# Kernel optimization log

Measured on AMD Instinct MI355X. Metric: run time of the kernel, lower is better.

Reference implementation:

```python
import jax, jax.numpy as jnp
import numpy as np

BOS_ID = 0
EOS_ID = 1


def setup_inputs() -> dict:
    key = jax.random.key(0)
    ks = jax.random.split(key, 16)
    B, L, F = 64, 200, 512
    H, E, A = 512, 512, 512
    V, T = 50257, 21
    D = E + F  # rnn input_dim
    s = lambda n: 1.0 / np.sqrt(n)
    ref = jax.random.randint(ks[0], (B, T), 2, V, dtype=jnp.int32)
    ref = ref.at[:, 0].set(BOS_ID).at[:, -1].set(EOS_ID)
    return {
        "encoder_output": jax.random.normal(ks[1], (B, L, F), jnp.float32),
        "decoder_init_hidden": jax.random.normal(ks[2], (1, B, H), jnp.float32),
        "encoding_mask": jnp.ones((B, L, 1), jnp.float32),
        "temp_seg": jax.random.uniform(ks[3], (B, 2), jnp.float32),
        "embed_table": jax.random.normal(ks[4], (V, E), jnp.float32) * 0.02,
        "W_ih": jax.random.normal(ks[5], (3 * H, D), jnp.float32) * s(D),
        "W_hh": jax.random.normal(ks[6], (3 * H, H), jnp.float32) * s(H),
        "b_ih": jnp.zeros((3 * H,), jnp.float32),
        "b_hh": jnp.zeros((3 * H,), jnp.float32),
        "Wa_enc": jax.random.normal(ks[7], (F, A), jnp.float32) * s(F),
        "Wa_h": jax.random.normal(ks[8], (H, A), jnp.float32) * s(H),
        "v_att": jax.random.normal(ks[9], (A,), jnp.float32) * s(A),
        "W_out": jax.random.normal(ks[10], (V, H), jnp.float32) * s(H),
        "b_out": jnp.zeros((V,), jnp.float32),
        "ref_caption": ref,
    }


def reference(encoder_output, decoder_init_hidden, encoding_mask, temp_seg,
              embed_table, W_ih, W_hh, b_ih, b_hh,
              Wa_enc, Wa_h, v_att, W_out, b_out, ref_caption):
    # Teacher-forced training forward of RNNSeqDecoder (GRU, 1 layer).
    B, T = ref_caption.shape
    V = embed_table.shape[0]
    enc_proj = jnp.einsum('blf,fa->bla', encoder_output, Wa_enc)  # precompute attn enc term
    mask = encoding_mask[..., 0]  # (B,L)
    h0 = decoder_init_hidden[0]   # (B,H)

    def step(h, word):
        emb = embed_table[word]                                        # (B,E)
        # additive attention over encoder states (masked)
        score = jnp.einsum('bla,a->bl', jnp.tanh(enc_proj + (h @ Wa_h)[:, None, :]), v_att)
        score = jnp.where(mask > 0, score, -1e9)
        attn = jax.nn.softmax(score, axis=1)
        ctx = jnp.einsum('bl,blf->bf', attn, encoder_output)           # (B,F)
        x = jnp.concatenate([emb, ctx], axis=1)                        # (B,E+F)
        # PyTorch GRU cell
        gi = x @ W_ih.T + b_ih
        gh = h @ W_hh.T + b_hh
        i_r, i_z, i_n = jnp.split(gi, 3, axis=1)
        h_r, h_z, h_n = jnp.split(gh, 3, axis=1)
        r = jax.nn.sigmoid(i_r + h_r)
        z = jax.nn.sigmoid(i_z + h_z)
        n = jnp.tanh(i_n + r * h_n)
        h_new = (1.0 - z) * n + z * h
        logp = jax.nn.log_softmax(h_new @ W_out.T + b_out, axis=1)     # (B,V)
        return h_new, logp

    _, logps = jax.lax.scan(step, h0, ref_caption[:, :-1].T)           # (T-1,B,V)
    first = jnp.zeros((B, 1, V), logps.dtype)  # BOS_ID == 0, matches torch.zeros(...) + BOS_ID
    caption_prob = jnp.concatenate([first, jnp.swapaxes(logps, 0, 1)], axis=1)  # (B,T,V)
    return caption_prob
```

## Files before the change

kernel.cpp:

```cpp
#include <hip/hip_runtime.h>
#include <stdint.h>
#include <stddef.h>

#define B_ 64
#define L_ 200
#define F_ 512
#define H_ 512
#define A_ 512
#define E_ 512
#define V_ 50257
#define PADV 50304
#define T_ 21
#define D_ 1024
#define NBLK_LOG 786
#define BH (B_ * H_)
#define BD (B_ * D_)
#define NROW 1280

typedef __attribute__((ext_vector_type(8))) short short8;
typedef __attribute__((ext_vector_type(4))) float f32x4;

__device__ __forceinline__ unsigned short f2b(float f) {
  unsigned int u = __builtin_bit_cast(unsigned int, f);
  u += 0x7FFFu + ((u >> 16) & 1u);
  return (unsigned short)(u >> 16);
}
__device__ __forceinline__ float b2f(unsigned short s) {
  unsigned int u = ((unsigned int)s) << 16;
  return __builtin_bit_cast(float, u);
}
__device__ __forceinline__ f32x4 mfma16(short8 a, short8 b, f32x4 c) {
  return __builtin_amdgcn_mfma_f32_16x16x32_bf16(a, b, c, 0, 0, 0);
}
__device__ __forceinline__ int hsoff(int b, int j) {
  return (((b >> 4) * 16 + (j >> 5)) * 64 + (((j >> 3) & 3) * 16 + (b & 15))) * 8 + (j & 7);
}
__device__ __forceinline__ int xoff(int b, int k) {
  return (((b >> 4) * 32 + (k >> 5)) * 64 + (((k >> 3) & 3) * 16 + (b & 15))) * 8 + (k & 7);
}


__global__ void k_cvt(const float* __restrict__ src, unsigned short* __restrict__ dst, int n4) {
  int i = blockIdx.x * blockDim.x + threadIdx.x;
  int stride = gridDim.x * blockDim.x;
  const float4* s4 = (const float4*)src;
  ushort4* d4 = (ushort4*)dst;
  for (; i < n4; i += stride) {
    float4 v = s4[i];
    ushort4 o;
    o.x = f2b(v.x); o.y = f2b(v.y); o.z = f2b(v.z); o.w = f2b(v.w);
    d4[i] = o;
  }
}

__global__ void k_wfrag(const float* __restrict__ src, unsigned short* __restrict__ dst, int K) {
  int rt = blockIdx.x;
  int r15 = threadIdx.x & 15;
  int row = rt * 16 + r15;
  int nch = K >> 3;
  int kpw = K >> 5;
  for (int kc = threadIdx.x >> 4; kc < nch; kc += 16) {
    const float4* s = (const float4*)(src + (size_t)row * K + kc * 8);
    float4 x = s[0], y = s[1];
    short8 o;
    o[0] = f2b(x.x); o[1] = f2b(x.y); o[2] = f2b(x.z); o[3] = f2b(x.w);
    o[4] = f2b(y.x); o[5] = f2b(y.y); o[6] = f2b(y.z); o[7] = f2b(y.w);
    *(short8*)(dst + ((size_t)(rt * kpw + (kc >> 2)) * 64 + ((kc & 3) * 16 + r15)) * 8) = o;
  }
}

__global__ void k_transcvt(const float* __restrict__ src, unsigned short* __restrict__ dst, int R, int C) {
  __shared__ float tile[64][65];
  int cb = blockIdx.x * 64, rb = blockIdx.y * 64;
  int tx = threadIdx.x & 63, ty = threadIdx.x >> 6;
#pragma unroll
  for (int i = 0; i < 16; ++i) {
    int r = ty * 16 + i;
    tile[r][tx] = src[(size_t)(rb + r) * C + cb + tx];
  }
  __syncthreads();
#pragma unroll
  for (int i = 0; i < 16; ++i) {
    int c = ty * 16 + i;
    dst[(size_t)(cb + c) * R + rb + tx] = f2b(tile[tx][c]);
  }
}

__global__ void k_trans32(const float* __restrict__ src, float* __restrict__ dst, int R, int C) {
  __shared__ float tile[64][65];
  int cb = blockIdx.x * 64, rb = blockIdx.y * 64;
  int tx = threadIdx.x & 63, ty = threadIdx.x >> 6;
#pragma unroll
  for (int i = 0; i < 16; ++i) {
    int r = ty * 16 + i;
    tile[r][tx] = src[(size_t)(rb + r) * C + cb + tx];
  }
  __syncthreads();
#pragma unroll
  for (int i = 0; i < 16; ++i) {
    int c = ty * 16 + i;
    dst[(size_t)(cb + c) * R + rb + tx] = tile[tx][c];
  }
}

__global__ void k_hs0(const float* __restrict__ src, unsigned short* __restrict__ hs) {
  int b = blockIdx.x;
  for (int j = threadIdx.x; j < H_; j += 256)
    hs[hsoff(b, j)] = f2b(src[(size_t)b * H_ + j]);
}

__global__ void k_embAll(const int* __restrict__ ref, const float* __restrict__ et,
                         unsigned short* __restrict__ xAll) {
  int b = blockIdx.x, tp = blockIdx.y;
  int word = ref[b * T_ + tp];
  const float* er = et + (size_t)word * E_;
  unsigned short* dst = xAll + (size_t)tp * BD;
  int c = threadIdx.x;
  const float4* s = (const float4*)(er + c * 8);
  float4 x = s[0], y = s[1];
  short8 o;
  o[0] = f2b(x.x); o[1] = f2b(x.y); o[2] = f2b(x.z); o[3] = f2b(x.w);
  o[4] = f2b(y.x); o[5] = f2b(y.y); o[6] = f2b(y.z); o[7] = f2b(y.w);
  *(short8*)(dst + xoff(b, c * 8)) = o;
}

__global__ __launch_bounds__(256, 2) void k_encproj2(const unsigned short* __restrict__ encb,
                                                     const unsigned short* __restrict__ WaTb,
                                                     unsigned short* __restrict__ epb) {
  __shared__ unsigned short al[32768];
  int tid = threadIdx.x;
  size_t rowbase = (size_t)blockIdx.x * 64;
  for (int idx = tid; idx < 4096; idx += 256) {
    int row = idx >> 6, seg = idx & 63;
    unsigned char* dp = (unsigned char*)al + row * 1024 + ((seg * 16) ^ ((row & 7) << 4));
    *(short8*)dp = *(const short8*)(encb + (rowbase + row) * F_ + seg * 8);
  }
  __syncthreads();
  int w = tid >> 6, lane = tid & 63, ln15 = lane & 15, g = lane >> 4;
  int sw = (ln15 & 7) << 4;
  const unsigned char* alb = (const unsigned char*)al;
  int mrow = w * 16 + ln15;
  for (int nt = 0; nt < 32; ++nt) {
    f32x4 acc = {0.f, 0.f, 0.f, 0.f};
    const unsigned short* brow = WaTb + (size_t)(nt * 16 + ln15) * F_ + 8 * g;
#pragma unroll 4
    for (int kk = 0; kk < 16; ++kk) {
      short8 bf = *(const short8*)(brow + kk * 32);
      short8 af = *(const short8*)(alb + mrow * 1024 + ((kk * 64 + 16 * g) ^ sw));
      acc = mfma16(af, bf, acc);
    }
#pragma unroll
    for (int r = 0; r < 4; ++r) {
      size_t m = rowbase + w * 16 + 4 * g + r;
      epb[m * A_ + nt * 16 + ln15] = f2b(acc[r]);
    }
  }
}

__global__ void k_zero0(float* __restrict__ out) {
  int b = blockIdx.y;
  float* o = out + (size_t)b * T_ * V_;
  int v0 = blockIdx.x * 1024 + threadIdx.x;
#pragma unroll
  for (int i = 0; i < 4; ++i) { int v = v0 + i * 256; if (v < V_) o[v] = 0.f; }
}


__global__ __launch_bounds__(256) void k_hw(const unsigned short* __restrict__ Wahf,
                                            const unsigned short* __restrict__ hs,
                                            float* __restrict__ hw) {
  int bx = blockIdx.x;
  int w = threadIdx.x >> 6, lane = threadIdx.x & 63;
  int ln15 = lane & 15, g = lane >> 4;
  f32x4 acc = {0.f, 0.f, 0.f, 0.f};
#pragma unroll 4
  for (int kk = 0; kk < 16; ++kk) {
    short8 av = *(const short8*)(Wahf + (((size_t)bx * 16 + kk) * 64 + lane) * 8);
    short8 hv = *(const short8*)(hs + (((size_t)w * 16 + kk) * 64 + lane) * 8);
    acc = mfma16(av, hv, acc);
  }
#pragma unroll
  for (int r = 0; r < 4; ++r) {
    int a = bx * 16 + 4 * g + r;
    int b = w * 16 + ln15;
    hw[(size_t)b * 512 + a] = acc[r];
  }
}


__global__ __launch_bounds__(1024) void k_attB(const float* __restrict__ mask,
                                               const float* __restrict__ vatt,
                                               const unsigned short* __restrict__ encb,
                                               const unsigned short* __restrict__ epb,
                                               const float* __restrict__ hw,
                                               unsigned short* __restrict__ xplane) {
  __shared__ float sm[208];
  __shared__ float ctxp[16][F_];
  __shared__ float ctxF[F_];
  int b = blockIdx.x;
  int tid = threadIdx.x;
  int w = tid >> 6, lane = tid & 63;
  float hwv[8], vv[8];
  {
    const float4* hp = (const float4*)(hw + (size_t)b * 512 + lane * 8);
    const float4* vp = (const float4*)(vatt + lane * 8);
    float4 h0 = hp[0], h1 = hp[1], v0 = vp[0], v1 = vp[1];
    hwv[0] = h0.x; hwv[1] = h0.y; hwv[2] = h0.z; hwv[3] = h0.w;
    hwv[4] = h1.x; hwv[5] = h1.y; hwv[6] = h1.z; hwv[7] = h1.w;
    vv[0] = v0.x; vv[1] = v0.y; vv[2] = v0.z; vv[3] = v0.w;
    vv[4] = v1.x; vv[5] = v1.y; vv[6] = v1.z; vv[7] = v1.w;
  }
  for (int l = w; l < L_; l += 16) {
    short8 ev = *(const short8*)(epb + ((size_t)(b * L_ + l)) * 512 + lane * 8);
    float p = 0.f;
#pragma unroll
    for (int j = 0; j < 8; ++j) {
      float x = b2f((unsigned short)ev[j]) + hwv[j];
      float e2 = __expf(x + x);
      p = fmaf(1.f - 2.f / (e2 + 1.f), vv[j], p);
    }
    for (int o = 1; o < 64; o <<= 1) p += __shfl_xor(p, o);
    if (lane == 0) {
      float mk = mask[b * L_ + l];
      sm[l] = (mk > 0.f) ? p : -1e9f;
    }
  }
  __syncthreads();
  if (tid < 64) {
    float m = -1e30f;
    for (int l = tid; l < L_; l += 64) m = fmaxf(m, sm[l]);
    for (int o = 1; o < 64; o <<= 1) m = fmaxf(m, __shfl_xor(m, o));
    float s = 0.f;
    for (int l = tid; l < L_; l += 64) s += __expf(sm[l] - m);
    for (int o = 1; o < 64; o <<= 1) s += __shfl_xor(s, o);
    float inv = 1.f / s;
    for (int l = tid; l < L_; l += 64) sm[l] = __expf(sm[l] - m) * inv;
  }
  __syncthreads();
  float c[8] = {0.f, 0.f, 0.f, 0.f, 0.f, 0.f, 0.f, 0.f};
  for (int l = w; l < L_; l += 16) {
    float wgt = sm[l];
    short8 ev = *(const short8*)(encb + ((size_t)(b * L_ + l)) * 512 + lane * 8);
#pragma unroll
    for (int j = 0; j < 8; ++j) c[j] = fmaf(wgt, b2f((unsigned short)ev[j]), c[j]);
  }
#pragma unroll
  for (int j = 0; j < 8; ++j) ctxp[w][lane * 8 + j] = c[j];
  __syncthreads();
  if (tid < 512) {
    float s = 0.f;
#pragma unroll
    for (int q = 0; q < 16; ++q) s += ctxp[q][tid];
    ctxF[tid] = s;
  }
  __syncthreads();
  if (tid < 64) {
    short8 o;
#pragma unroll
    for (int j = 0; j < 8; ++j) o[j] = f2b(ctxF[tid * 8 + j]);
    *(short8*)(xplane + xoff(b, E_ + tid * 8)) = o;
  }
}


__global__ __launch_bounds__(256) void k_gruM(const unsigned short* __restrict__ Wfih,
                                              const unsigned short* __restrict__ Wfhh,
                                              const float* __restrict__ bih,
                                              const float* __restrict__ bhh,
                                              const unsigned short* __restrict__ xplane,
                                              const unsigned short* __restrict__ hsold,
                                              const float* __restrict__ hTold,
                                              unsigned short* __restrict__ hsnew,
                                              float* __restrict__ hTnew) {
  int bx = blockIdx.x;
  int w = threadIdx.x >> 6, lane = threadIdx.x & 63;
  int ln15 = lane & 15, g = lane >> 4;
  f32x4 z4 = {0.f, 0.f, 0.f, 0.f};
  f32x4 aIr = z4, aIz = z4, aIn = z4, aHr = z4, aHz = z4, aHn = z4;
  {
#pragma unroll 2
    for (int kk = 0; kk < 32; ++kk) {
      short8 xv = *(const short8*)(xplane + (((size_t)w * 32 + kk) * 64 + lane) * 8);
      aIr = mfma16(*(const short8*)(Wfih + (((size_t)(0 * 32 + bx) * 32 + kk) * 64 + lane) * 8), xv, aIr);
      aIz = mfma16(*(const short8*)(Wfih + (((size_t)(32 + bx) * 32 + kk) * 64 + lane) * 8), xv, aIz);
      aIn = mfma16(*(const short8*)(Wfih + (((size_t)(64 + bx) * 32 + kk) * 64 + lane) * 8), xv, aIn);
    }
  }
  {
#pragma unroll 2
    for (int kk = 0; kk < 16; ++kk) {
      short8 hv = *(const short8*)(hsold + (((size_t)w * 16 + kk) * 64 + lane) * 8);
      aHr = mfma16(*(const short8*)(Wfhh + (((size_t)(0 * 32 + bx) * 16 + kk) * 64 + lane) * 8), hv, aHr);
      aHz = mfma16(*(const short8*)(Wfhh + (((size_t)(32 + bx) * 16 + kk) * 64 + lane) * 8), hv, aHz);
      aHn = mfma16(*(const short8*)(Wfhh + (((size_t)(64 + bx) * 16 + kk) * 64 + lane) * 8), hv, aHn);
    }
  }
  int jb = bx * 16;
#pragma unroll
  for (int r = 0; r < 4; ++r) {
    int j = jb + 4 * g + r;
    int b = w * 16 + ln15;
    float ir = aIr[r] + bih[j];
    float iz = aIz[r] + bih[512 + j];
    float in_ = aIn[r] + bih[1024 + j];
    float hrv = aHr[r] + bhh[j];
    float hzv = aHz[r] + bhh[512 + j];
    float hnv = aHn[r] + bhh[1024 + j];
    float rg = 1.f / (1.f + __expf(-(ir + hrv)));
    float zg = 1.f / (1.f + __expf(-(iz + hzv)));
    float e2 = __expf(2.f * (in_ + rg * hnv));
    float ng = 1.f - 2.f / (e2 + 1.f);
    float ho = hTold[(size_t)j * B_ + b];
    float hv = (1.f - zg) * ng + zg * ho;
    hTnew[(size_t)j * B_ + b] = hv;
    hsnew[hsoff(b, j)] = f2b(hv);
  }
}


__global__ __launch_bounds__(256) void k_blog(const unsigned short* __restrict__ Wb,
                                              const float* __restrict__ bout,
                                              const unsigned short* __restrict__ hsAll,
                                              float* __restrict__ pm, float* __restrict__ ps,
                                              float* __restrict__ out,
                                              unsigned short* __restrict__ lws, int mode) {
  __shared__ float tile[64][68];
  __shared__ float redm[64][4], reds[64][4];
  int tid = threadIdx.x;
  int w = tid >> 6, lane = tid & 63, ln15 = lane & 15, g = lane >> 4;
  int vcol = blockIdx.x * 64 + w * 16 + ln15;
  bool vok = vcol < V_;
  int vr = vok ? vcol : (V_ - 1);
  const unsigned short* brow = Wb + (size_t)vr * H_ + 8 * g;
  short8 wb[16];
#pragma unroll
  for (int kk = 0; kk < 16; ++kk) wb[kk] = *(const short8*)(brow + kk * 32);
  float bo = bout[vr];
  int row = tid >> 2, seg = tid & 3;

  for (int t = 0; t < T_ - 1; ++t) {
    const unsigned short* hp = hsAll + (size_t)(t + 1) * BH;
#pragma unroll
    for (int mp = 0; mp < 2; ++mp) {
      f32x4 z4 = {0.f, 0.f, 0.f, 0.f};
      f32x4 acc0 = z4, acc1 = z4;
#pragma unroll
      for (int kk = 0; kk < 16; ++kk) {
        short8 a0 = *(const short8*)(hp + (((mp * 2 + 0) * 16 + kk) * 64 + lane) * 8);
        short8 a1 = *(const short8*)(hp + (((mp * 2 + 1) * 16 + kk) * 64 + lane) * 8);
        acc0 = mfma16(a0, wb[kk], acc0);
        acc1 = mfma16(a1, wb[kk], acc1);
      }
#pragma unroll
      for (int r = 0; r < 4; ++r) {
        int bi0 = (mp * 2 + 0) * 16 + 4 * g + r;
        int bi1 = (mp * 2 + 1) * 16 + 4 * g + r;
        tile[bi0][w * 16 + ln15] = vok ? acc0[r] + bo : -1e30f;
        tile[bi1][w * 16 + ln15] = vok ? acc1[r] + bo : -1e30f;
      }
    }
    __syncthreads();
    float v[16];
#pragma unroll
    for (int q = 0; q < 4; ++q) {
      float4 fv = *(const float4*)&tile[row][seg * 16 + q * 4];
      v[q * 4 + 0] = fv.x; v[q * 4 + 1] = fv.y; v[q * 4 + 2] = fv.z; v[q * 4 + 3] = fv.w;
    }
    int cb = blockIdx.x * 64 + seg * 16;
    if (mode == 1) {
      unsigned short* orow = lws + ((size_t)t * 64 + row) * PADV + cb;
      short8 o0, o1;
#pragma unroll
      for (int i = 0; i < 8; ++i) { o0[i] = f2b(v[i]); o1[i] = f2b(v[8 + i]); }
      *(short8*)orow = o0;
      *(short8*)(orow + 8) = o1;
    } else {
      float* orow = out + ((size_t)row * T_ + (t + 1)) * V_ + cb;
      if (cb + 16 <= V_) {
#pragma unroll
        for (int q = 0; q < 4; ++q)
          *(float4*)(orow + q * 4) = make_float4(v[q * 4], v[q * 4 + 1], v[q * 4 + 2], v[q * 4 + 3]);
      } else {
        for (int i = 0; i < 16; ++i)
          if (cb + i < V_) orow[i] = v[i];
      }
    }
    float m = -1e30f;
#pragma unroll
    for (int i = 0; i < 16; ++i) m = fmaxf(m, v[i]);
    float s = 0.f;
#pragma unroll
    for (int i = 0; i < 16; ++i) s += __expf(v[i] - m);
    redm[row][seg] = m; reds[row][seg] = s;
    __syncthreads();
    if (seg == 0) {
      float m0 = redm[row][0], m1 = redm[row][1], m2 = redm[row][2], m3 = redm[row][3];
      float m4 = fmaxf(fmaxf(m0, m1), fmaxf(m2, m3));
      float s4 = reds[row][0] * __expf(m0 - m4) + reds[row][1] * __expf(m1 - m4) +
                 reds[row][2] * __expf(m2 - m4) + reds[row][3] * __expf(m3 - m4);
      size_t rho = (size_t)t * 64 + row;
      pm[rho * NBLK_LOG + blockIdx.x] = m4;
      ps[rho * NBLK_LOG + blockIdx.x] = s4;
    }
  }
}

__global__ __launch_bounds__(256) void k_lse(const float* __restrict__ pm,
                                             const float* __restrict__ ps,
                                             float* __restrict__ lse) {
  int rho = blockIdx.x;
  int tid = threadIdx.x;
  float m = -1e30f, s = 0.f;
  for (int p = tid; p < NBLK_LOG; p += 256) {
    float pmv = pm[(size_t)rho * NBLK_LOG + p], psv = ps[(size_t)rho * NBLK_LOG + p];
    float nm = fmaxf(m, pmv);
    s = s * __expf(m - nm) + psv * __expf(pmv - nm);
    m = nm;
  }
  __shared__ float lm[256], ls[256];
  lm[tid] = m; ls[tid] = s;
  __syncthreads();
  for (int o = 128; o > 0; o >>= 1) {
    if (tid < o) {
      float m2 = lm[tid + o], s2 = ls[tid + o];
      float nm = fmaxf(lm[tid], m2);
      ls[tid] = ls[tid] * __expf(lm[tid] - nm) + s2 * __expf(m2 - nm);
      lm[tid] = nm;
    }
    __syncthreads();
  }
  if (tid == 0) lse[rho] = lm[0] + logf(ls[0]);
}

__global__ __launch_bounds__(256) void k_fin(float* __restrict__ out, const float* __restrict__ lse) {
  int rho = blockIdx.x;
  int tp = rho >> 6, b = rho & 63;
  float Lv = lse[rho];
  float* o = out + ((size_t)b * T_ + (tp + 1)) * V_;
  float4* o4 = (float4*)o;
  int tid = threadIdx.x;
  for (int i = tid; i < 12564; i += 256) {
    float4 v = o4[i];
    v.x -= Lv; v.y -= Lv; v.z -= Lv; v.w -= Lv;
    o4[i] = v;
  }
  if (tid == 0) o[50256] -= Lv;
}

__global__ __launch_bounds__(256) void k_finb(const unsigned short* __restrict__ lws,
                                              const float* __restrict__ lse,
                                              float* __restrict__ out) {
  int rho = blockIdx.x;
  int tp = rho >> 6, b = rho & 63;
  float Lv = lse[rho];
  const unsigned short* src = lws + (size_t)(tp * 64 + b) * PADV;
  float* o = out + ((size_t)b * T_ + (tp + 1)) * V_;
  int tid = threadIdx.x;
  for (int i = tid; i < 6282; i += 256) {
    short8 sv = *(const short8*)(src + i * 8);
    float4 v0, v1;
    v0.x = b2f((unsigned short)sv[0]) - Lv; v0.y = b2f((unsigned short)sv[1]) - Lv;
    v0.z = b2f((unsigned short)sv[2]) - Lv; v0.w = b2f((unsigned short)sv[3]) - Lv;
    v1.x = b2f((unsigned short)sv[4]) - Lv; v1.y = b2f((unsigned short)sv[5]) - Lv;
    v1.z = b2f((unsigned short)sv[6]) - Lv; v1.w = b2f((unsigned short)sv[7]) - Lv;
    *(float4*)(o + i * 8) = v0;
    *(float4*)(o + i * 8 + 4) = v1;
  }
  if (tid == 0) o[50256] = b2f(src[50256]) - Lv;
}


extern "C" void kernel_launch(void* const* d_in, const int* in_sizes, int n_in,
                              void* d_out, int out_size, void* d_ws, size_t ws_size,
                              hipStream_t stream) {
  const float* enc   = (const float*)d_in[0];
  const float* dih   = (const float*)d_in[1];
  const float* mask  = (const float*)d_in[2];
  const float* et    = (const float*)d_in[4];
  const float* Wih   = (const float*)d_in[5];
  const float* Whh   = (const float*)d_in[6];
  const float* bih   = (const float*)d_in[7];
  const float* bhh   = (const float*)d_in[8];
  const float* Waenc = (const float*)d_in[9];
  const float* Wah   = (const float*)d_in[10];
  const float* vatt  = (const float*)d_in[11];
  const float* Wout  = (const float*)d_in[12];
  const float* bout  = (const float*)d_in[13];
  const int*   ref   = (const int*)d_in[14];
  float* out = (float*)d_out;

  char* w = (char*)d_ws;
  size_t o = 0;
  unsigned short* Wb    = (unsigned short*)(w + o); o += (size_t)V_ * H_ * 2;
  unsigned short* Wfih  = (unsigned short*)(w + o); o += (size_t)1536 * 1024 * 2;
  unsigned short* Wfhh  = (unsigned short*)(w + o); o += (size_t)1536 * 512 * 2;
  unsigned short* WaTb  = (unsigned short*)(w + o); o += (size_t)512 * 512 * 2;
  unsigned short* Wahf  = (unsigned short*)(w + o); o += (size_t)512 * 512 * 2;
  float* WahT32 = (float*)(w + o); o += (size_t)512 * 512 * 4;
  unsigned short* encb  = (unsigned short*)(w + o); o += (size_t)B_ * L_ * F_ * 2;
  unsigned short* epb   = (unsigned short*)(w + o); o += (size_t)B_ * L_ * A_ * 2;
  unsigned short* xAll  = (unsigned short*)(w + o); o += (size_t)20 * BD * 2;
  unsigned short* hsAll = (unsigned short*)(w + o); o += (size_t)T_ * BH * 2;
  float* hTAll = (float*)(w + o); o += (size_t)T_ * BH * 4;
  float* hw    = (float*)(w + o); o += (size_t)B_ * A_ * 4;
  float* pm  = (float*)(w + o); o += (size_t)NROW * NBLK_LOG * 4;
  float* ps  = (float*)(w + o); o += (size_t)NROW * NBLK_LOG * 4;
  float* lse = (float*)(w + o); o += (size_t)NROW * 4 + 256;
  unsigned short* lws = (unsigned short*)(w + o);
  size_t need = o + (size_t)NROW * PADV * 2;
  int mode = (ws_size >= need) ? 1 : 0;

  k_cvt<<<4096, 256, 0, stream>>>(Wout, Wb, V_ * H_ / 4);
  k_cvt<<<2048, 256, 0, stream>>>(enc, encb, B_ * L_ * F_ / 4);
  k_wfrag<<<96, 256, 0, stream>>>(Wih, Wfih, 1024);
  k_wfrag<<<96, 256, 0, stream>>>(Whh, Wfhh, 512);
  k_transcvt<<<dim3(8, 8), 256, 0, stream>>>(Waenc, WaTb, 512, 512);
  k_trans32<<<dim3(8, 8), 256, 0, stream>>>(Wah, WahT32, 512, 512);
  k_wfrag<<<32, 256, 0, stream>>>(WahT32, Wahf, 512);
  k_trans32<<<dim3(8, 1), 256, 0, stream>>>(dih, hTAll, 64, 512);
  k_hs0<<<64, 256, 0, stream>>>(dih, hsAll);
  k_embAll<<<dim3(64, 20), 64, 0, stream>>>(ref, et, xAll);
  k_encproj2<<<200, 256, 0, stream>>>(encb, WaTb, epb);
  k_zero0<<<dim3(50, 64), 256, 0, stream>>>(out);

  for (int t = 0; t < T_ - 1; ++t) {
    const float* hT_t = hTAll + (size_t)t * BH;
    float* hT_n = hTAll + (size_t)(t + 1) * BH;
    const unsigned short* hs_t = hsAll + (size_t)t * BH;
    unsigned short* hs_n = hsAll + (size_t)(t + 1) * BH;
    unsigned short* xp = xAll + (size_t)t * BD;
    k_hw<<<32, 256, 0, stream>>>(Wahf, hs_t, hw);
    k_attB<<<64, 1024, 0, stream>>>(mask, vatt, encb, epb, hw, xp);
    k_gruM<<<32, 256, 0, stream>>>(Wfih, Wfhh, bih, bhh, xp, hs_t, hT_t, hs_n, hT_n);
  }
  k_blog<<<NBLK_LOG, 256, 0, stream>>>(Wb, bout, hsAll, pm, ps, out, lws, mode);
  k_lse<<<1280, 256, 0, stream>>>(pm, ps, lse);
  if (mode == 1) k_finb<<<1280, 256, 0, stream>>>(lws, lse, out);
  else k_fin<<<1280, 256, 0, stream>>>(out, lse);
}
```

Measured before the change: 1.466 ms.

## Move hidden-gate GEMM into attention-prep kernel, widen logits blocks, split finalize

```diff
diff --git a/kernel.cpp b/kernel.cpp
--- a/kernel.cpp
+++ b/kernel.cpp
@@ -166,24 +166,47 @@
 }
 
 
-__global__ __launch_bounds__(256) void k_hw(const unsigned short* __restrict__ Wahf,
-                                            const unsigned short* __restrict__ hs,
-                                            float* __restrict__ hw) {
-  int bx = blockIdx.x;
+__global__ __launch_bounds__(256) void k_hwgh(const unsigned short* __restrict__ Wahf,
+                                              const unsigned short* __restrict__ Wfhh,
+                                              const unsigned short* __restrict__ hs,
+                                              float* __restrict__ hw,
+                                              float* __restrict__ ghG) {
+  int blk = blockIdx.x;
   int w = threadIdx.x >> 6, lane = threadIdx.x & 63;
   int ln15 = lane & 15, g = lane >> 4;
-  f32x4 acc = {0.f, 0.f, 0.f, 0.f};
+  if (blk < 32) {
+    f32x4 acc = {0.f, 0.f, 0.f, 0.f};
 #pragma unroll 4
-  for (int kk = 0; kk < 16; ++kk) {
-    short8 av = *(const short8*)(Wahf + (((size_t)bx * 16 + kk) * 64 + lane) * 8);
-    short8 hv = *(const short8*)(hs + (((size_t)w * 16 + kk) * 64 + lane) * 8);
-    acc = mfma16(av, hv, acc);
-  }
-#pragma unroll
-  for (int r = 0; r < 4; ++r) {
-    int a = bx * 16 + 4 * g + r;
-    int b = w * 16 + ln15;
-    hw[(size_t)b * 512 + a] = acc[r];
+    for (int kk = 0; kk < 16; ++kk) {
+      short8 av = *(const short8*)(Wahf + (((size_t)blk * 16 + kk) * 64 + lane) * 8);
+      short8 hv = *(const short8*)(hs + (((size_t)w * 16 + kk) * 64 + lane) * 8);
+      acc = mfma16(av, hv, acc);
+    }
+#pragma unroll
+    for (int r = 0; r < 4; ++r) {
+      int a = blk * 16 + 4 * g + r;
+      int b = w * 16 + ln15;
+      hw[(size_t)b * 512 + a] = acc[r];
+    }
+  } else {
+    int base = (blk - 32) * 3;
+#pragma unroll
+    for (int i = 0; i < 3; ++i) {
+      int jt = base + i;
+      f32x4 acc = {0.f, 0.f, 0.f, 0.f};
+#pragma unroll
+      for (int kk = 0; kk < 16; ++kk) {
+        short8 wv = *(const short8*)(Wfhh + (((size_t)jt * 16 + kk) * 64 + lane) * 8);
+        short8 hv = *(const short8*)(hs + (((size_t)w * 16 + kk) * 64 + lane) * 8);
+        acc = mfma16(wv, hv, acc);
+      }
+#pragma unroll
+      for (int r = 0; r < 4; ++r) {
+        int j = jt * 16 + 4 * g + r;
+        int b = w * 16 + ln15;
+        ghG[(size_t)j * B_ + b] = acc[r];
+      }
+    }
   }
 }
 
@@ -263,37 +286,25 @@
 }
 
 
-__global__ __launch_bounds__(256) void k_gruM(const unsigned short* __restrict__ Wfih,
-                                              const unsigned short* __restrict__ Wfhh,
-                                              const float* __restrict__ bih,
-                                              const float* __restrict__ bhh,
-                                              const unsigned short* __restrict__ xplane,
-                                              const unsigned short* __restrict__ hsold,
-                                              const float* __restrict__ hTold,
-                                              unsigned short* __restrict__ hsnew,
-                                              float* __restrict__ hTnew) {
+__global__ __launch_bounds__(256) void k_stepB(const unsigned short* __restrict__ Wfih,
+                                               const float* __restrict__ bih,
+                                               const float* __restrict__ bhh,
+                                               const unsigned short* __restrict__ xplane,
+                                               const float* __restrict__ ghG,
+                                               const float* __restrict__ hBold,
+                                               unsigned short* __restrict__ hsnew,
+                                               float* __restrict__ hBnew) {
   int bx = blockIdx.x;
   int w = threadIdx.x >> 6, lane = threadIdx.x & 63;
   int ln15 = lane & 15, g = lane >> 4;
   f32x4 z4 = {0.f, 0.f, 0.f, 0.f};
-  f32x4 aIr = z4, aIz = z4, aIn = z4, aHr = z4, aHz = z4, aHn = z4;
-  {
+  f32x4 aIr = z4, aIz = z4, aIn = z4;
 #pragma unroll 2
-    for (int kk = 0; kk < 32; ++kk) {
-      short8 xv = *(const short8*)(xplane + (((size_t)w * 32 + kk) * 64 + lane) * 8);
-      aIr = mfma16(*(const short8*)(Wfih + (((size_t)(0 * 32 + bx) * 32 + kk) * 64 + lane) * 8), xv, aIr);
-      aIz = mfma16(*(const short8*)(Wfih + (((size_t)(32 + bx) * 32 + kk) * 64 + lane) * 8), xv, aIz);
-      aIn = mfma16(*(const short8*)(Wfih + (((size_t)(64 + bx) * 32 + kk) * 64 + lane) * 8), xv, aIn);
-    }
-  }
-  {
-#pragma unroll 2
-    for (int kk = 0; kk < 16; ++kk) {
-      short8 hv = *(const short8*)(hsold + (((size_t)w * 16 + kk) * 64 + lane) * 8);
-      aHr = mfma16(*(const short8*)(Wfhh + (((size_t)(0 * 32 + bx) * 16 + kk) * 64 + lane) * 8), hv, aHr);
-      aHz = mfma16(*(const short8*)(Wfhh + (((size_t)(32 + bx) * 16 + kk) * 64 + lane) * 8), hv, aHz);
-      aHn = mfma16(*(const short8*)(Wfhh + (((size_t)(64 + bx) * 16 + kk) * 64 + lane) * 8), hv, aHn);
-    }
+  for (int kk = 0; kk < 32; ++kk) {
+    short8 xv = *(const short8*)(xplane + (((size_t)w * 32 + kk) * 64 + lane) * 8);
+    aIr = mfma16(*(const short8*)(Wfih + (((size_t)(0 * 32 + bx) * 32 + kk) * 64 + lane) * 8), xv, aIr);
+    aIz = mfma16(*(const short8*)(Wfih + (((size_t)(32 + bx) * 32 + kk) * 64 + lane) * 8), xv, aIz);
+    aIn = mfma16(*(const short8*)(Wfih + (((size_t)(64 + bx) * 32 + kk) * 64 + lane) * 8), xv, aIn);
   }
   int jb = bx * 16;
 #pragma unroll
@@ -303,32 +314,33 @@
     float ir = aIr[r] + bih[j];
     float iz = aIz[r] + bih[512 + j];
     float in_ = aIn[r] + bih[1024 + j];
-    float hrv = aHr[r] + bhh[j];
-    float hzv = aHz[r] + bhh[512 + j];
-    float hnv = aHn[r] + bhh[1024 + j];
+    float hrv = ghG[(size_t)j * B_ + b] + bhh[j];
+    float hzv = ghG[(size_t)(512 + j) * B_ + b] + bhh[512 + j];
+    float hnv = ghG[(size_t)(1024 + j) * B_ + b] + bhh[1024 + j];
     float rg = 1.f / (1.f + __expf(-(ir + hrv)));
     float zg = 1.f / (1.f + __expf(-(iz + hzv)));
     float e2 = __expf(2.f * (in_ + rg * hnv));
     float ng = 1.f - 2.f / (e2 + 1.f);
-    float ho = hTold[(size_t)j * B_ + b];
+    float ho = hBold[(size_t)b * H_ + j];
     float hv = (1.f - zg) * ng + zg * ho;
-    hTnew[(size_t)j * B_ + b] = hv;
+    hBnew[(size_t)b * H_ + j] = hv;
     hsnew[hsoff(b, j)] = f2b(hv);
   }
 }
 
 
-__global__ __launch_bounds__(256) void k_blog(const unsigned short* __restrict__ Wb,
+__global__ __launch_bounds__(512) void k_blog(const unsigned short* __restrict__ Wb,
                                               const float* __restrict__ bout,
                                               const unsigned short* __restrict__ hsAll,
                                               float* __restrict__ pm, float* __restrict__ ps,
                                               float* __restrict__ out,
                                               unsigned short* __restrict__ lws, int mode) {
   __shared__ float tile[64][68];
-  __shared__ float redm[64][4], reds[64][4];
+  __shared__ float redm[64][8], reds[64][8];
   int tid = threadIdx.x;
   int w = tid >> 6, lane = tid & 63, ln15 = lane & 15, g = lane >> 4;
-  int vcol = blockIdx.x * 64 + w * 16 + ln15;
+  int vt = w & 3, mh = w >> 2;
+  int vcol = blockIdx.x * 64 + vt * 16 + ln15;
   bool vok = vcol < V_;
   int vr = vok ? vcol : (V_ - 1);
   const unsigned short* brow = Wb + (size_t)vr * H_ + 8 * g;
@@ -336,72 +348,69 @@
 #pragma unroll
   for (int kk = 0; kk < 16; ++kk) wb[kk] = *(const short8*)(brow + kk * 32);
   float bo = bout[vr];
-  int row = tid >> 2, seg = tid & 3;
+  int row = tid >> 3, s8 = tid & 7;
 
   for (int t = 0; t < T_ - 1; ++t) {
     const unsigned short* hp = hsAll + (size_t)(t + 1) * BH;
 #pragma unroll
     for (int mp = 0; mp < 2; ++mp) {
-      f32x4 z4 = {0.f, 0.f, 0.f, 0.f};
-      f32x4 acc0 = z4, acc1 = z4;
+      int mt = mh * 2 + mp;
+      f32x4 acc = {0.f, 0.f, 0.f, 0.f};
 #pragma unroll
       for (int kk = 0; kk < 16; ++kk) {
-        short8 a0 = *(const short8*)(hp + (((mp * 2 + 0) * 16 + kk) * 64 + lane) * 8);
-        short8 a1 = *(const short8*)(hp + (((mp * 2 + 1) * 16 + kk) * 64 + lane) * 8);
-        acc0 = mfma16(a0, wb[kk], acc0);
-        acc1 = mfma16(a1, wb[kk], acc1);
+        short8 a0 = *(const short8*)(hp + (((size_t)(mt * 16 + kk)) * 64 + lane) * 8);
+        acc = mfma16(a0, wb[kk], acc);
       }
 #pragma unroll
       for (int r = 0; r < 4; ++r) {
-        int bi0 = (mp * 2 + 0) * 16 + 4 * g + r;
-        int bi1 = (mp * 2 + 1) * 16 + 4 * g + r;
-        tile[bi0][w * 16 + ln15] = vok ? acc0[r] + bo : -1e30f;
-        tile[bi1][w * 16 + ln15] = vok ? acc1[r] + bo : -1e30f;
+        int bi = mt * 16 + 4 * g + r;
+        tile[bi][vt * 16 + ln15] = vok ? acc[r] + bo : -1e30f;
       }
     }
     __syncthreads();
-    float v[16];
-#pragma unroll
-    for (int q = 0; q < 4; ++q) {
-      float4 fv = *(const float4*)&tile[row][seg * 16 + q * 4];
+    float v[8];
+#pragma unroll
+    for (int q = 0; q < 2; ++q) {
+      float4 fv = *(const float4*)&tile[row][s8 * 8 + q * 4];
       v[q * 4 + 0] = fv.x; v[q * 4 + 1] = fv.y; v[q * 4 + 2] = fv.z; v[q * 4 + 3] = fv.w;
     }
-    int cb = blockIdx.x * 64 + seg * 16;
+    int cb = blockIdx.x * 64 + s8 * 8;
     if (mode == 1) {
       unsigned short* orow = lws + ((size_t)t * 64 + row) * PADV + cb;
-      short8 o0, o1;
-#pragma unroll
-      for (int i = 0; i < 8; ++i) { o0[i] = f2b(v[i]); o1[i] = f2b(v[8 + i]); }
+      short8 o0;
+#pragma unroll
+      for (int i = 0; i < 8; ++i) o0[i] = f2b(v[i]);
       *(short8*)orow = o0;
-      *(short8*)(orow + 8) = o1;
     } else {
       float* orow = out + ((size_t)row * T_ + (t + 1)) * V_ + cb;
-      if (cb + 16 <= V_) {
-#pragma unroll
-        for (int q = 0; q < 4; ++q)
-          *(float4*)(orow + q * 4) = make_float4(v[q * 4], v[q * 4 + 1], v[q * 4 + 2], v[q * 4 + 3]);
+      if (cb + 8 <= V_) {
+#pragma unroll
+        for (int i = 0; i < 8; ++i) orow[i] = v[i];
       } else {
-        for (int i = 0; i < 16; ++i)
+        for (int i = 0; i < 8; ++i)
           if (cb + i < V_) orow[i] = v[i];
       }
     }
     float m = -1e30f;
 #pragma unroll
-    for (int i = 0; i < 16; ++i) m = fmaxf(m, v[i]);
+    for (int i = 0; i < 8; ++i) m = fmaxf(m, v[i]);
     float s = 0.f;
 #pragma unroll
-    for (int i = 0; i < 16; ++i) s += __expf(v[i] - m);
-    redm[row][seg] = m; reds[row][seg] = s;
+    for (int i = 0; i < 8; ++i) s += __expf(v[i] - m);
+    redm[row][s8] = m; reds[row][s8] = s;
     __syncthreads();
-    if (seg == 0) {
-      float m0 = redm[row][0], m1 = redm[row][1], m2 = redm[row][2], m3 = redm[row][3];
-      float m4 = fmaxf(fmaxf(m0, m1), fmaxf(m2, m3));
-      float s4 = reds[row][0] * __expf(m0 - m4) + reds[row][1] * __expf(m1 - m4) +
-                 reds[row][2] * __expf(m2 - m4) + reds[row][3] * __expf(m3 - m4);
+    if (s8 == 0) {
+      float m4 = -1e30f;
+#pragma unroll
+      for (int i = 0; i < 8; ++i) m4 = fmaxf(m4, redm[row][i]);
+      float s4 = 0.f;
+#pragma unroll
+      for (int i = 0; i < 8; ++i) s4 += reds[row][i] * __expf(redm[row][i] - m4);
       size_t rho = (size_t)t * 64 + row;
       pm[rho * NBLK_LOG + blockIdx.x] = m4;
       ps[rho * NBLK_LOG + blockIdx.x] = s4;
     }
+    __syncthreads();
   }
 }
 
@@ -437,9 +446,9 @@
   int tp = rho >> 6, b = rho & 63;
   float Lv = lse[rho];
   float* o = out + ((size_t)b * T_ + (tp + 1)) * V_;
-  float4* o4 = (float4*)o;
   int tid = threadIdx.x;
   for (int i = tid; i < 12564; i += 256) {
+    float4* o4 = (float4*)o;
     float4 v = o4[i];
     v.x -= Lv; v.y -= Lv; v.z -= Lv; v.w -= Lv;
     o4[i] = v;
@@ -450,13 +459,15 @@
 __global__ __launch_bounds__(256) void k_finb(const unsigned short* __restrict__ lws,
                                               const float* __restrict__ lse,
                                               float* __restrict__ out) {
-  int rho = blockIdx.x;
+  int rho = blockIdx.x >> 1;
+  int half = blockIdx.x & 1;
   int tp = rho >> 6, b = rho & 63;
   float Lv = lse[rho];
   const unsigned short* src = lws + (size_t)(tp * 64 + b) * PADV;
   float* o = out + ((size_t)b * T_ + (tp + 1)) * V_;
   int tid = threadIdx.x;
-  for (int i = tid; i < 6282; i += 256) {
+  int i0 = half * 3141, i1 = i0 + 3141;
+  for (int i = i0 + tid; i < i1; i += 256) {
     short8 sv = *(const short8*)(src + i * 8);
     float4 v0, v1;
     v0.x = b2f((unsigned short)sv[0]) - Lv; v0.y = b2f((unsigned short)sv[1]) - Lv;
@@ -466,7 +477,7 @@
     *(float4*)(o + i * 8) = v0;
     *(float4*)(o + i * 8 + 4) = v1;
   }
-  if (tid == 0) o[50256] = b2f(src[50256]) - Lv;
+  if (half == 1 && tid == 0) o[50256] = b2f(src[50256]) - Lv;
 }
 
 
@@ -501,7 +512,8 @@
   unsigned short* epb   = (unsigned short*)(w + o); o += (size_t)B_ * L_ * A_ * 2;
   unsigned short* xAll  = (unsigned short*)(w + o); o += (size_t)20 * BD * 2;
   unsigned short* hsAll = (unsigned short*)(w + o); o += (size_t)T_ * BH * 2;
-  float* hTAll = (float*)(w + o); o += (size_t)T_ * BH * 4;
+  float* hBAll = (float*)(w + o); o += (size_t)T_ * BH * 4;
+  float* ghG   = (float*)(w + o); o += (size_t)1536 * B_ * 4;
   float* hw    = (float*)(w + o); o += (size_t)B_ * A_ * 4;
   float* pm  = (float*)(w + o); o += (size_t)NROW * NBLK_LOG * 4;
   float* ps  = (float*)(w + o); o += (size_t)NROW * NBLK_LOG * 4;
@@ -517,24 +529,23 @@
   k_transcvt<<<dim3(8, 8), 256, 0, stream>>>(Waenc, WaTb, 512, 512);
   k_trans32<<<dim3(8, 8), 256, 0, stream>>>(Wah, WahT32, 512, 512);
   k_wfrag<<<32, 256, 0, stream>>>(WahT32, Wahf, 512);
-  k_trans32<<<dim3(8, 1), 256, 0, stream>>>(dih, hTAll, 64, 512);
   k_hs0<<<64, 256, 0, stream>>>(dih, hsAll);
   k_embAll<<<dim3(64, 20), 64, 0, stream>>>(ref, et, xAll);
   k_encproj2<<<200, 256, 0, stream>>>(encb, WaTb, epb);
   k_zero0<<<dim3(50, 64), 256, 0, stream>>>(out);
 
   for (int t = 0; t < T_ - 1; ++t) {
-    const float* hT_t = hTAll + (size_t)t * BH;
-    float* hT_n = hTAll + (size_t)(t + 1) * BH;
+    const float* hB_t = (t == 0) ? dih : (hBAll + (size_t)t * BH);
+    float* hB_n = hBAll + (size_t)(t + 1) * BH;
     const unsigned short* hs_t = hsAll + (size_t)t * BH;
     unsigned short* hs_n = hsAll + (size_t)(t + 1) * BH;
     unsigned short* xp = xAll + (size_t)t * BD;
-    k_hw<<<32, 256, 0, stream>>>(Wahf, hs_t, hw);
+    k_hwgh<<<64, 256, 0, stream>>>(Wahf, Wfhh, hs_t, hw, ghG);
     k_attB<<<64, 1024, 0, stream>>>(mask, vatt, encb, epb, hw, xp);
-    k_gruM<<<32, 256, 0, stream>>>(Wfih, Wfhh, bih, bhh, xp, hs_t, hT_t, hs_n, hT_n);
-  }
-  k_blog<<<NBLK_LOG, 256, 0, stream>>>(Wb, bout, hsAll, pm, ps, out, lws, mode);
+    k_stepB<<<32, 256, 0, stream>>>(Wfih, bih, bhh, xp, ghG, hB_t, hs_n, hB_n);
+  }
+  k_blog<<<NBLK_LOG, 512, 0, stream>>>(Wb, bout, hsAll, pm, ps, out, lws, mode);
   k_lse<<<1280, 256, 0, stream>>>(pm, ps, lse);
-  if (mode == 1) k_finb<<<1280, 256, 0, stream>>>(lws, lse, out);
+  if (mode == 1) k_finb<<<2560, 256, 0, stream>>>(lws, lse, out);
   else k_fin<<<1280, 256, 0, stream>>>(out, lse);
 }
```

New measurement: 1.504 ms. 2.6% more time.
